# Performance work log

Measured on AMD Instinct MI355X. Metric: run time of the kernel, lower is better.

Reference implementation:

```python
import jax, jax.numpy as jnp
import numpy as np

B, T, D, H = 4, 2048, 1024, 16
DK = D // H  # 64


def setup_inputs() -> dict:
    key = jax.random.key(0)
    ks = jax.random.split(key, 8)
    std = 1.0 / np.sqrt(2.0 * D)  # initialize_weights: normal(0, 1/sqrt(2*d_model*(i_layer+1))), i_layer=0
    inp = {
        "q": jax.random.normal(ks[0], (B, T, D), jnp.float32),
        "k": jax.random.normal(ks[1], (B, T, D), jnp.float32),
        "v": jax.random.normal(ks[2], (B, T, D), jnp.float32),
        "Wq": jax.random.normal(ks[3], (D, D), jnp.float32) * std,
        "Wk": jax.random.normal(ks[4], (D, D), jnp.float32) * std,
        "Wv": jax.random.normal(ks[5], (D, D), jnp.float32) * std,
        "Wo": jax.random.normal(ks[6], (D, D), jnp.float32) * std,
        "bq": jnp.zeros((D,), jnp.float32),
        "bk": jnp.zeros((D,), jnp.float32),
        "bv": jnp.zeros((D,), jnp.float32),
        "bo": jnp.zeros((D,), jnp.float32),
    }
    return inp


def _split_heads(x):
    # (B,T,D) -> (B,H,T,DK), same as x.view(B,T,H,DK).transpose(1,2)
    b, t, _ = x.shape
    return x.reshape(b, t, H, DK).transpose(0, 2, 1, 3)


def reference(q, k, v, Wq, Wk, Wv, Wo, bq, bk, bv, bo):
    # Linear projections (torch Linear: x @ W.T + b)
    qh = _split_heads(q @ Wq.T + bq)  # (B,H,T,DK)
    kh = _split_heads(k @ Wk.T + bk)
    vh = _split_heads(v @ Wv.T + bv)

    # scaled dot-product similarities: (B,H,Tq,Tk)
    scores = jnp.einsum("bhqd,bhkd->bhqk", qh, kh) / jnp.sqrt(jnp.float32(DK))

    # causal mask: tril(ones)==0 positions filled with -inf
    tq, tk = scores.shape[-2], scores.shape[-1]
    causal = jnp.tril(jnp.ones((tq, tk), dtype=bool))
    scores = jnp.where(causal, scores, jnp.float32(-jnp.inf))

    attn = jax.nn.softmax(scores, axis=-1)  # (B,H,Tq,Tk)
    ctx = jnp.einsum("bhqk,bhkd->bhqd", attn, vh)  # (B,H,Tq,DK)

    # merge heads: (B,H,T,DK) -> (B,T,D), then output projection
    merged = ctx.transpose(0, 2, 1, 3).reshape(q.shape[0], tq, D)
    return merged @ Wo.T + bo
```

## Files before the change

kernel.cpp:

```cpp
#include <hip/hip_runtime.h>
#include <hip/hip_bf16.h>
#include <stdint.h>

#define B_ 4
#define T_ 2048
#define D_ 1024
#define H_ 16
#define DK_ 64
#define M_ (B_*T_)

typedef __attribute__((ext_vector_type(8))) short bf16x8;
typedef __attribute__((ext_vector_type(4))) short bf16x4;
typedef __attribute__((ext_vector_type(4))) float f32x4;
typedef __hip_bfloat16 bf16;

__device__ __forceinline__ void gld_lds16(const bf16* g, bf16* l) {
  __builtin_amdgcn_global_load_lds((const __attribute__((address_space(1))) void*)g,
                                   (__attribute__((address_space(3))) void*)l,
                                   16, 0, 0);
}

__device__ __forceinline__ short bfbits(float f) {
  union { bf16 h; short s; } u; u.h = __float2bfloat16(f); return u.s;
}

__global__ __launch_bounds__(256) void cvt_all(
    const float* __restrict__ q, const float* __restrict__ k, const float* __restrict__ v,
    const float* __restrict__ wq, const float* __restrict__ wk,
    const float* __restrict__ wv, const float* __restrict__ wo,
    bf16* __restrict__ qb, bf16* __restrict__ kb, bf16* __restrict__ vb,
    bf16* __restrict__ wqb, bf16* __restrict__ wkb,
    bf16* __restrict__ wvb, bf16* __restrict__ wob) {
  int gid = blockIdx.x * 256 + threadIdx.x;
  const float* src; bf16* dst; int off;
  if (gid < 6291456) {
    int s = gid >> 21; off = gid & 2097151;
    src = (s == 0) ? q : (s == 1) ? k : v;
    dst = (s == 0) ? qb : (s == 1) ? kb : vb;
  } else {
    int g2 = gid - 6291456;
    int s = g2 >> 18; off = g2 & 262143;
    src = (s == 0) ? wq : (s == 1) ? wk : (s == 2) ? wv : wo;
    dst = (s == 0) ? wqb : (s == 1) ? wkb : (s == 2) ? wvb : wob;
  }
  float4 val = reinterpret_cast<const float4*>(src)[off];
  union { ushort4 u; bf16 h[4]; } o;
  o.h[0] = __float2bfloat16(val.x);
  o.h[1] = __float2bfloat16(val.y);
  o.h[2] = __float2bfloat16(val.z);
  o.h[3] = __float2bfloat16(val.w);
  reinterpret_cast<ushort4*>(dst)[off] = o.u;
}

__global__ __launch_bounds__(256) void proj_qkv(
    const bf16* __restrict__ qb, const bf16* __restrict__ kb, const bf16* __restrict__ vb,
    const bf16* __restrict__ Wqb, const bf16* __restrict__ Wkb, const bf16* __restrict__ Wvb,
    const float* __restrict__ bq, const float* __restrict__ bk, const float* __restrict__ bv,
    bf16* __restrict__ Qh, bf16* __restrict__ Kh, bf16* __restrict__ Vt) {
  constexpr int K = 1024;
  constexpr int BK = 64;
  __shared__ __align__(16) bf16 As[128 * BK];
  __shared__ __align__(16) bf16 Bs[128 * BK];

  const int z = blockIdx.z;
  const bool vt = (z == 2);
  const bf16* A  = (z == 0) ? qb : (z == 1) ? kb : Wvb;
  const bf16* Bm = (z == 0) ? Wqb : (z == 1) ? Wkb : vb;
  const float* bias = (z == 0) ? bq : (z == 1) ? bk : bv;
  bf16* out = (z == 0) ? Qh : (z == 1) ? Kh : Vt;
  const float scale = (z == 0) ? 0.125f * 1.4426950408889634f : 1.0f;

  const int bm = vt ? blockIdx.y : blockIdx.x;
  const int bn = vt ? blockIdx.x : blockIdx.y;

  const int tid = threadIdx.x;
  const int w = tid >> 6, l = tid & 63;
  const int wr = w >> 1, wc = w & 1;
  const int lr = l & 15, lk = l >> 4;

  f32x4 acc[4][4] = {};

  for (int k0 = 0; k0 < K; k0 += BK) {
#pragma unroll
    for (int i = 0; i < 4; ++i) {
      int p = i * 256 + tid;
      int row = p >> 3;
      int so = (p & 7) ^ (row & 7);
      gld_lds16(A + (size_t)(bm * 128 + row) * K + k0 + so * 8, &As[p * 8]);
    }
#pragma unroll
    for (int i = 0; i < 4; ++i) {
      int p = i * 256 + tid;
      int row = p >> 3;
      int so = (p & 7) ^ (row & 7);
      gld_lds16(Bm + (size_t)(bn * 128 + row) * K + k0 + so * 8, &Bs[p * 8]);
    }
    __syncthreads();

#pragma unroll
    for (int kk = 0; kk < 2; ++kk) {
      bf16x8 af[4], bfr[4];
#pragma unroll
      for (int m = 0; m < 4; ++m) {
        int row = wr * 64 + m * 16 + lr;
        int slot = (kk * 4 + lk) ^ (row & 7);
        af[m] = *reinterpret_cast<const bf16x8*>(&As[row * BK + slot * 8]);
      }
#pragma unroll
      for (int n = 0; n < 4; ++n) {
        int row = wc * 64 + n * 16 + lr;
        int slot = (kk * 4 + lk) ^ (row & 7);
        bfr[n] = *reinterpret_cast<const bf16x8*>(&Bs[row * BK + slot * 8]);
      }
#pragma unroll
      for (int m = 0; m < 4; ++m)
#pragma unroll
        for (int n = 0; n < 4; ++n)
          acc[m][n] = __builtin_amdgcn_mfma_f32_16x16x32_bf16(af[m], bfr[n], acc[m][n], 0, 0, 0);
    }
    __syncthreads();
  }

  const int crow0 = bm * 128 + wr * 64;
  const int ccol0 = bn * 128 + wc * 64;
#pragma unroll
  for (int m = 0; m < 4; ++m) {
#pragma unroll
    for (int n = 0; n < 4; ++n) {
#pragma unroll
      for (int r = 0; r < 4; ++r) {
        const int row = crow0 + m * 16 + lk * 4 + r;
        const int col = ccol0 + n * 16 + lr;
        if (!vt) {
          float vv = (acc[m][n][r] + bias[col]) * scale;
          size_t idx = (((size_t)(row >> 11) * H_ + (col >> 6)) * T_ + (row & (T_ - 1))) * DK_ + (col & (DK_ - 1));
          out[idx] = __float2bfloat16(vv);
        } else {
          float vv = acc[m][n][r] + bias[row];
          size_t idx = (size_t)(col >> 11) * ((size_t)H_ * DK_ * T_) + (size_t)row * T_ + (col & (T_ - 1));
          out[idx] = __float2bfloat16(vv);
        }
      }
    }
  }
}

__global__ __launch_bounds__(256) void gemm_out(const bf16* __restrict__ A,
                                                const bf16* __restrict__ Bm,
                                                const float* __restrict__ bias,
                                                float* __restrict__ Cout) {
  constexpr int K = 1024;
  constexpr int BK = 64;
  __shared__ __align__(16) bf16 As[128 * BK];
  __shared__ __align__(16) bf16 Bs[128 * BK];

  const int bm = blockIdx.x;
  const int bn = blockIdx.y;
  const int tid = threadIdx.x;
  const int w = tid >> 6, l = tid & 63;
  const int wr = w >> 1, wc = w & 1;
  const int lr = l & 15, lk = l >> 4;

  f32x4 acc[4][4] = {};

  for (int k0 = 0; k0 < K; k0 += BK) {
#pragma unroll
    for (int i = 0; i < 4; ++i) {
      int p = i * 256 + tid;
      int row = p >> 3;
      int so = (p & 7) ^ (row & 7);
      gld_lds16(A + (size_t)(bm * 128 + row) * K + k0 + so * 8, &As[p * 8]);
    }
#pragma unroll
    for (int i = 0; i < 4; ++i) {
      int p = i * 256 + tid;
      int row = p >> 3;
      int so = (p & 7) ^ (row & 7);
      gld_lds16(Bm + (size_t)(bn * 128 + row) * K + k0 + so * 8, &Bs[p * 8]);
    }
    __syncthreads();

#pragma unroll
    for (int kk = 0; kk < 2; ++kk) {
      bf16x8 af[4], bfr[4];
#pragma unroll
      for (int m = 0; m < 4; ++m) {
        int row = wr * 64 + m * 16 + lr;
        int slot = (kk * 4 + lk) ^ (row & 7);
        af[m] = *reinterpret_cast<const bf16x8*>(&As[row * BK + slot * 8]);
      }
#pragma unroll
      for (int n = 0; n < 4; ++n) {
        int row = wc * 64 + n * 16 + lr;
        int slot = (kk * 4 + lk) ^ (row & 7);
        bfr[n] = *reinterpret_cast<const bf16x8*>(&Bs[row * BK + slot * 8]);
      }
#pragma unroll
      for (int m = 0; m < 4; ++m)
#pragma unroll
        for (int n = 0; n < 4; ++n)
          acc[m][n] = __builtin_amdgcn_mfma_f32_16x16x32_bf16(af[m], bfr[n], acc[m][n], 0, 0, 0);
    }
    __syncthreads();
  }

  const int crow0 = bm * 128 + wr * 64;
  const int ccol0 = bn * 128 + wc * 64;
#pragma unroll
  for (int m = 0; m < 4; ++m) {
#pragma unroll
    for (int n = 0; n < 4; ++n) {
#pragma unroll
      for (int r = 0; r < 4; ++r) {
        const int row = crow0 + m * 16 + lk * 4 + r;
        const int col = ccol0 + n * 16 + lr;
        Cout[(size_t)row * D_ + col] = acc[m][n][r] + bias[col];
      }
    }
  }
}

__global__ __launch_bounds__(256, 2) void attn_fwd(const bf16* __restrict__ Qh,
                                                   const bf16* __restrict__ Kh,
                                                   const bf16* __restrict__ Vt,
                                                   bf16* __restrict__ ctx) {
  __shared__ __align__(16) bf16 Kbuf[2][128 * 64];
  __shared__ __align__(16) bf16 Vbuf[2][64 * 128];
  __shared__ __align__(16) char Ps[4][16 * 256];

  const int tid = threadIdx.x, w = tid >> 6, l = tid & 63;
  const int lr = l & 15, lk = l >> 4;
  const int bid = blockIdx.x;
  const int xcd = bid & 7, local = bid >> 3;
  const int hsub = local >> 4;
  const int pp = local & 15;
  char* Pw = &Ps[w][0];

#pragma unroll 1
  for (int ph = 0; ph < 2; ++ph) {
    const int head = xcd * 8 + ph * 4 + hsub;
    const bf16* Qb = Qh + (size_t)head * T_ * DK_;
    const bf16* Kb = Kh + (size_t)head * T_ * DK_;
    const bf16* Vb = Vt + (size_t)head * DK_ * T_;
    const int bb = head >> 4, hh = head & 15;

#pragma unroll 1
    for (int ti = 0; ti < 2; ++ti) {
      const int t = ti ? (31 - pp) : pp;
      const int r0 = t * 64;
      const int ntiles = (t + 2) >> 1;
      const int qrow = r0 + w * 16 + lr;

      const bf16* qp = Qb + (size_t)qrow * DK_ + lk * 8;
      bf16x8 qf0 = *reinterpret_cast<const bf16x8*>(qp);
      bf16x8 qf1 = *reinterpret_cast<const bf16x8*>(qp + 32);

      f32x4 oacc[4] = {};
      float mrow = -1e30f, srow = 0.f;

#pragma unroll
      for (int i = 0; i < 4; ++i) {
        int p = i * 256 + tid;
        int row = p >> 3;
        int so = (p & 7) ^ (row & 7);
        gld_lds16(Kb + (size_t)row * DK_ + so * 8, &Kbuf[0][p * 8]);
      }
#pragma unroll
      for (int i = 0; i < 4; ++i) {
        int p = i * 256 + tid;
        int row = p >> 4;
        int so = (p & 15) ^ (row & 15);
        gld_lds16(Vb + (size_t)row * T_ + so * 8, &Vbuf[0][p * 8]);
      }
      __syncthreads();

      int buf = 0;
#pragma unroll 1
      for (int j = 0; j < ntiles; ++j) {
        const int k0 = j * 128;
        if (j + 1 < ntiles) {
          const int k0n = k0 + 128;
#pragma unroll
          for (int i = 0; i < 4; ++i) {
            int p = i * 256 + tid;
            int row = p >> 3;
            int so = (p & 7) ^ (row & 7);
            gld_lds16(Kb + (size_t)(k0n + row) * DK_ + so * 8, &Kbuf[buf ^ 1][p * 8]);
          }
#pragma unroll
          for (int i = 0; i < 4; ++i) {
            int p = i * 256 + tid;
            int row = p >> 4;
            int so = (p & 15) ^ (row & 15);
            gld_lds16(Vb + (size_t)row * T_ + k0n + so * 8, &Vbuf[buf ^ 1][p * 8]);
          }
        }

        f32x4 sacc[8];
        __builtin_amdgcn_s_setprio(1);
#pragma unroll
        for (int n = 0; n < 8; ++n) {
          int row = n * 16 + lr;
          int s0 = lk ^ (row & 7);
          int s1 = (4 + lk) ^ (row & 7);
          bf16x8 kf0 = *reinterpret_cast<const bf16x8*>(&Kbuf[buf][row * 64 + s0 * 8]);
          bf16x8 kf1 = *reinterpret_cast<const bf16x8*>(&Kbuf[buf][row * 64 + s1 * 8]);
          sacc[n] = f32x4{0.f, 0.f, 0.f, 0.f};
          sacc[n] = __builtin_amdgcn_mfma_f32_16x16x32_bf16(kf0, qf0, sacc[n], 0, 0, 0);
          sacc[n] = __builtin_amdgcn_mfma_f32_16x16x32_bf16(kf1, qf1, sacc[n], 0, 0, 0);
        }
        __builtin_amdgcn_s_setprio(0);

        if (j == ntiles - 1) {
#pragma unroll
          for (int n = 0; n < 8; ++n)
#pragma unroll
            for (int r = 0; r < 4; ++r)
              if (k0 + n * 16 + lk * 4 + r > qrow) sacc[n][r] = -1e30f;
        }

        float pm = -1e30f;
#pragma unroll
        for (int n = 0; n < 8; ++n)
          pm = fmaxf(pm, fmaxf(fmaxf(sacc[n][0], sacc[n][1]), fmaxf(sacc[n][2], sacc[n][3])));
        pm = fmaxf(pm, __shfl_xor(pm, 16, 64));
        pm = fmaxf(pm, __shfl_xor(pm, 32, 64));

        if (!__all(pm - mrow <= 8.0f)) {
          const float mn = fmaxf(mrow, pm);
          const float sc = __builtin_exp2f(mrow - mn);
          mrow = mn;
          srow *= sc;
#pragma unroll
          for (int n = 0; n < 4; ++n)
#pragma unroll
            for (int r = 0; r < 4; ++r)
              oacc[n][r] *= sc;
        }

        float ts = 0.f;
#pragma unroll
        for (int n = 0; n < 8; ++n) {
          float p0 = __builtin_exp2f(sacc[n][0] - mrow);
          float p1 = __builtin_exp2f(sacc[n][1] - mrow);
          float p2 = __builtin_exp2f(sacc[n][2] - mrow);
          float p3 = __builtin_exp2f(sacc[n][3] - mrow);
          ts += (p0 + p1) + (p2 + p3);
          bf16x4 pk;
          pk[0] = bfbits(p0); pk[1] = bfbits(p1); pk[2] = bfbits(p2); pk[3] = bfbits(p3);
          int swz = (n * 2 + (lk >> 1)) ^ (lr & 15);
          *reinterpret_cast<bf16x4*>(Pw + lr * 256 + swz * 16 + (lk & 1) * 8) = pk;
        }
        ts += __shfl_xor(ts, 16, 64);
        ts += __shfl_xor(ts, 32, 64);
        srow += ts;

        bf16x8 pa[4];
#pragma unroll
        for (int kb2 = 0; kb2 < 4; ++kb2) {
          int swz = (kb2 * 4 + lk) ^ (lr & 15);
          pa[kb2] = *reinterpret_cast<const bf16x8*>(Pw + lr * 256 + swz * 16);
        }

        __builtin_amdgcn_s_setprio(1);
#pragma unroll
        for (int n = 0; n < 4; ++n) {
          int row = n * 16 + lr;
#pragma unroll
          for (int kb2 = 0; kb2 < 4; ++kb2) {
            int sl = (kb2 * 4 + lk) ^ (row & 15);
            bf16x8 vf = *reinterpret_cast<const bf16x8*>(&Vbuf[buf][row * 128 + sl * 8]);
            oacc[n] = __builtin_amdgcn_mfma_f32_16x16x32_bf16(vf, pa[kb2], oacc[n], 0, 0, 0);
          }
        }
        __builtin_amdgcn_s_setprio(0);

        __syncthreads();
        buf ^= 1;
      }

      const float inv = 1.0f / srow;
#pragma unroll
      for (int n = 0; n < 4; ++n) {
        bf16x4 pk;
#pragma unroll
        for (int r = 0; r < 4; ++r) pk[r] = bfbits(oacc[n][r] * inv);
        *reinterpret_cast<bf16x4*>(&ctx[((size_t)(bb * T_ + qrow)) * D_ + hh * DK_ + n * 16 + lk * 4]) = pk;
      }
      __syncthreads();
    }
  }
}

extern "C" void kernel_launch(void* const* d_in, const int* in_sizes, int n_in,
                              void* d_out, int out_size, void* d_ws, size_t ws_size,
                              hipStream_t stream) {
  const float* q  = (const float*)d_in[0];
  const float* k  = (const float*)d_in[1];
  const float* v  = (const float*)d_in[2];
  const float* Wq = (const float*)d_in[3];
  const float* Wk = (const float*)d_in[4];
  const float* Wv = (const float*)d_in[5];
  const float* Wo = (const float*)d_in[6];
  const float* bq = (const float*)d_in[7];
  const float* bk = (const float*)d_in[8];
  const float* bv = (const float*)d_in[9];
  const float* bo = (const float*)d_in[10];

  constexpr size_t E_IN = (size_t)M_ * D_;
  constexpr size_t E_W  = (size_t)D_ * D_;
  char* ws = (char*)d_ws;
  size_t off = 0;
  bf16* qb  = (bf16*)(ws + off); off += E_IN * 2;
  bf16* kb  = (bf16*)(ws + off); off += E_IN * 2;
  bf16* vb  = (bf16*)(ws + off); off += E_IN * 2;
  bf16* Wqb = (bf16*)(ws + off); off += E_W * 2;
  bf16* Wkb = (bf16*)(ws + off); off += E_W * 2;
  bf16* Wvb = (bf16*)(ws + off); off += E_W * 2;
  bf16* Wob = (bf16*)(ws + off); off += E_W * 2;
  bf16* Qh  = (bf16*)(ws + off); off += E_IN * 2;
  bf16* Kh  = (bf16*)(ws + off); off += E_IN * 2;
  bf16* Vtw = (bf16*)(ws + off); off += E_IN * 2;
  bf16* ctx = (bf16*)(ws + off); off += E_IN * 2;

  cvt_all<<<dim3(28672), dim3(256), 0, stream>>>(q, k, v, Wq, Wk, Wv, Wo,
                                                 qb, kb, vb, Wqb, Wkb, Wvb, Wob);

  proj_qkv<<<dim3(64, 8, 3), dim3(256), 0, stream>>>(qb, kb, vb, Wqb, Wkb, Wvb,
                                                     bq, bk, bv, Qh, Kh, Vtw);

  attn_fwd<<<dim3(512), dim3(256), 0, stream>>>(Qh, Kh, Vtw, ctx);

  gemm_out<<<dim3(64, 8), dim3(256), 0, stream>>>(ctx, Wob, bo, (float*)d_out);
}
```

Measured before the change: 225.8 us.

## Shrink attention KV tiles to 64 and double grid for higher occupancy

The attention kernel now processes 64-key tiles instead of 128, halving LDS buffers for K, V and P, and raises launch bounds to 4 blocks per CU. The per-block loop over two heads is removed and the grid is doubled to 1024 blocks, with one head per block. The intent is more concurrent waves to hide latency and finer causal masking granularity, at the cost of more loop iterations, barriers and per-tile softmax overhead.

```diff
diff --git a/kernel.cpp b/kernel.cpp
--- a/kernel.cpp
+++ b/kernel.cpp
@@ -220,13 +220,13 @@
   }
 }
 
-__global__ __launch_bounds__(256, 2) void attn_fwd(const bf16* __restrict__ Qh,
+__global__ __launch_bounds__(256, 4) void attn_fwd(const bf16* __restrict__ Qh,
                                                    const bf16* __restrict__ Kh,
                                                    const bf16* __restrict__ Vt,
                                                    bf16* __restrict__ ctx) {
-  __shared__ __align__(16) bf16 Kbuf[2][128 * 64];
-  __shared__ __align__(16) bf16 Vbuf[2][64 * 128];
-  __shared__ __align__(16) char Ps[4][16 * 256];
+  __shared__ __align__(16) bf16 Kbuf[2][64 * 64];
+  __shared__ __align__(16) bf16 Vbuf[2][64 * 64];
+  __shared__ __align__(16) char Ps[4][16 * 128];
 
   const int tid = threadIdx.x, w = tid >> 6, l = tid & 63;
   const int lr = l & 15, lk = l >> 4;
@@ -236,159 +236,138 @@
   const int pp = local & 15;
   char* Pw = &Ps[w][0];
 
+  const int head = xcd * 8 + hsub;
+  const bf16* Qb = Qh + (size_t)head * T_ * DK_;
+  const bf16* Kb = Kh + (size_t)head * T_ * DK_;
+  const bf16* Vb = Vt + (size_t)head * DK_ * T_;
+  const int bb = head >> 4, hh = head & 15;
+
 #pragma unroll 1
-  for (int ph = 0; ph < 2; ++ph) {
-    const int head = xcd * 8 + ph * 4 + hsub;
-    const bf16* Qb = Qh + (size_t)head * T_ * DK_;
-    const bf16* Kb = Kh + (size_t)head * T_ * DK_;
-    const bf16* Vb = Vt + (size_t)head * DK_ * T_;
-    const int bb = head >> 4, hh = head & 15;
-
+  for (int ti = 0; ti < 2; ++ti) {
+    const int t = ti ? (31 - pp) : pp;
+    const int r0 = t * 64;
+    const int ntiles = t + 1;
+    const int qrow = r0 + w * 16 + lr;
+
+    const bf16* qp = Qb + (size_t)qrow * DK_ + lk * 8;
+    bf16x8 qf0 = *reinterpret_cast<const bf16x8*>(qp);
+    bf16x8 qf1 = *reinterpret_cast<const bf16x8*>(qp + 32);
+
+    f32x4 oacc[4] = {};
+    float mrow = -1e30f, srow = 0.f;
+
+#pragma unroll
+    for (int i = 0; i < 2; ++i) {
+      int p = i * 256 + tid;
+      int row = p >> 3;
+      int so = (p & 7) ^ (row & 7);
+      gld_lds16(Kb + (size_t)row * DK_ + so * 8, &Kbuf[0][p * 8]);
+      gld_lds16(Vb + (size_t)row * T_ + so * 8, &Vbuf[0][p * 8]);
+    }
+    __syncthreads();
+
+    int buf = 0;
 #pragma unroll 1
-    for (int ti = 0; ti < 2; ++ti) {
-      const int t = ti ? (31 - pp) : pp;
-      const int r0 = t * 64;
-      const int ntiles = (t + 2) >> 1;
-      const int qrow = r0 + w * 16 + lr;
-
-      const bf16* qp = Qb + (size_t)qrow * DK_ + lk * 8;
-      bf16x8 qf0 = *reinterpret_cast<const bf16x8*>(qp);
-      bf16x8 qf1 = *reinterpret_cast<const bf16x8*>(qp + 32);
-
-      f32x4 oacc[4] = {};
-      float mrow = -1e30f, srow = 0.f;
-
-#pragma unroll
-      for (int i = 0; i < 4; ++i) {
-        int p = i * 256 + tid;
-        int row = p >> 3;
-        int so = (p & 7) ^ (row & 7);
-        gld_lds16(Kb + (size_t)row * DK_ + so * 8, &Kbuf[0][p * 8]);
-      }
-#pragma unroll
-      for (int i = 0; i < 4; ++i) {
-        int p = i * 256 + tid;
-        int row = p >> 4;
-        int so = (p & 15) ^ (row & 15);
-        gld_lds16(Vb + (size_t)row * T_ + so * 8, &Vbuf[0][p * 8]);
-      }
+    for (int j = 0; j < ntiles; ++j) {
+      if (j + 1 < ntiles) {
+        const int k0n = (j + 1) * 64;
+#pragma unroll
+        for (int i = 0; i < 2; ++i) {
+          int p = i * 256 + tid;
+          int row = p >> 3;
+          int so = (p & 7) ^ (row & 7);
+          gld_lds16(Kb + (size_t)(k0n + row) * DK_ + so * 8, &Kbuf[buf ^ 1][p * 8]);
+          gld_lds16(Vb + (size_t)row * T_ + k0n + so * 8, &Vbuf[buf ^ 1][p * 8]);
+        }
+      }
+
+      f32x4 sacc[4] = {};
+      __builtin_amdgcn_s_setprio(1);
+#pragma unroll
+      for (int n = 0; n < 4; ++n) {
+        int row = n * 16 + lr;
+        int s0 = lk ^ (row & 7);
+        int s1 = (4 + lk) ^ (row & 7);
+        bf16x8 kf0 = *reinterpret_cast<const bf16x8*>(&Kbuf[buf][row * 64 + s0 * 8]);
+        bf16x8 kf1 = *reinterpret_cast<const bf16x8*>(&Kbuf[buf][row * 64 + s1 * 8]);
+        sacc[n] = __builtin_amdgcn_mfma_f32_16x16x32_bf16(kf0, qf0, sacc[n], 0, 0, 0);
+        sacc[n] = __builtin_amdgcn_mfma_f32_16x16x32_bf16(kf1, qf1, sacc[n], 0, 0, 0);
+      }
+      __builtin_amdgcn_s_setprio(0);
+
+      if (j == ntiles - 1) {
+#pragma unroll
+        for (int n = 0; n < 4; ++n)
+#pragma unroll
+          for (int r = 0; r < 4; ++r)
+            if (j * 64 + n * 16 + lk * 4 + r > qrow) sacc[n][r] = -1e30f;
+      }
+
+      float pm = fmaxf(fmaxf(sacc[0][0], sacc[0][1]), fmaxf(sacc[0][2], sacc[0][3]));
+#pragma unroll
+      for (int n = 1; n < 4; ++n)
+        pm = fmaxf(pm, fmaxf(fmaxf(sacc[n][0], sacc[n][1]), fmaxf(sacc[n][2], sacc[n][3])));
+      pm = fmaxf(pm, __shfl_xor(pm, 16, 64));
+      pm = fmaxf(pm, __shfl_xor(pm, 32, 64));
+
+      if (!__all(pm - mrow <= 8.0f)) {
+        const float mn = fmaxf(mrow, pm);
+        const float sc = __builtin_exp2f(mrow - mn);
+        mrow = mn;
+        srow *= sc;
+#pragma unroll
+        for (int n = 0; n < 4; ++n)
+#pragma unroll
+          for (int r = 0; r < 4; ++r)
+            oacc[n][r] *= sc;
+      }
+
+      float ts = 0.f;
+#pragma unroll
+      for (int n = 0; n < 4; ++n) {
+        float p0 = __builtin_exp2f(sacc[n][0] - mrow);
+        float p1 = __builtin_exp2f(sacc[n][1] - mrow);
+        float p2 = __builtin_exp2f(sacc[n][2] - mrow);
+        float p3 = __builtin_exp2f(sacc[n][3] - mrow);
+        ts += (p0 + p1) + (p2 + p3);
+        bf16x4 pk;
+        pk[0] = bfbits(p0); pk[1] = bfbits(p1); pk[2] = bfbits(p2); pk[3] = bfbits(p3);
+        int swz = (n * 2 + (lk >> 1)) ^ (lr & 7);
+        *reinterpret_cast<bf16x4*>(Pw + lr * 128 + swz * 16 + (lk & 1) * 8) = pk;
+      }
+      ts += __shfl_xor(ts, 16, 64);
+      ts += __shfl_xor(ts, 32, 64);
+      srow += ts;
+
+      bf16x8 pa0 = *reinterpret_cast<const bf16x8*>(Pw + lr * 128 + ((lk ^ (lr & 7)) << 4));
+      bf16x8 pa1 = *reinterpret_cast<const bf16x8*>(Pw + lr * 128 + (((4 + lk) ^ (lr & 7)) << 4));
+
+      __builtin_amdgcn_s_setprio(1);
+#pragma unroll
+      for (int n = 0; n < 4; ++n) {
+        int row = n * 16 + lr;
+        int s0 = lk ^ (row & 7);
+        int s1 = (4 + lk) ^ (row & 7);
+        bf16x8 vf0 = *reinterpret_cast<const bf16x8*>(&Vbuf[buf][row * 64 + s0 * 8]);
+        bf16x8 vf1 = *reinterpret_cast<const bf16x8*>(&Vbuf[buf][row * 64 + s1 * 8]);
+        oacc[n] = __builtin_amdgcn_mfma_f32_16x16x32_bf16(vf0, pa0, oacc[n], 0, 0, 0);
+        oacc[n] = __builtin_amdgcn_mfma_f32_16x16x32_bf16(vf1, pa1, oacc[n], 0, 0, 0);
+      }
+      __builtin_amdgcn_s_setprio(0);
+
       __syncthreads();
-
-      int buf = 0;
-#pragma unroll 1
-      for (int j = 0; j < ntiles; ++j) {
-        const int k0 = j * 128;
-        if (j + 1 < ntiles) {
-          const int k0n = k0 + 128;
-#pragma unroll
-          for (int i = 0; i < 4; ++i) {
-            int p = i * 256 + tid;
-            int row = p >> 3;
-            int so = (p & 7) ^ (row & 7);
-            gld_lds16(Kb + (size_t)(k0n + row) * DK_ + so * 8, &Kbuf[buf ^ 1][p * 8]);
-          }
-#pragma unroll
-          for (int i = 0; i < 4; ++i) {
-            int p = i * 256 + tid;
-            int row = p >> 4;
-            int so = (p & 15) ^ (row & 15);
-            gld_lds16(Vb + (size_t)row * T_ + k0n + so * 8, &Vbuf[buf ^ 1][p * 8]);
-          }
-        }
-
-        f32x4 sacc[8];
-        __builtin_amdgcn_s_setprio(1);
-#pragma unroll
-        for (int n = 0; n < 8; ++n) {
-          int row = n * 16 + lr;
-          int s0 = lk ^ (row & 7);
-          int s1 = (4 + lk) ^ (row & 7);
-          bf16x8 kf0 = *reinterpret_cast<const bf16x8*>(&Kbuf[buf][row * 64 + s0 * 8]);
-          bf16x8 kf1 = *reinterpret_cast<const bf16x8*>(&Kbuf[buf][row * 64 + s1 * 8]);
-          sacc[n] = f32x4{0.f, 0.f, 0.f, 0.f};
-          sacc[n] = __builtin_amdgcn_mfma_f32_16x16x32_bf16(kf0, qf0, sacc[n], 0, 0, 0);
-          sacc[n] = __builtin_amdgcn_mfma_f32_16x16x32_bf16(kf1, qf1, sacc[n], 0, 0, 0);
-        }
-        __builtin_amdgcn_s_setprio(0);
-
-        if (j == ntiles - 1) {
-#pragma unroll
-          for (int n = 0; n < 8; ++n)
-#pragma unroll
-            for (int r = 0; r < 4; ++r)
-              if (k0 + n * 16 + lk * 4 + r > qrow) sacc[n][r] = -1e30f;
-        }
-
-        float pm = -1e30f;
-#pragma unroll
-        for (int n = 0; n < 8; ++n)
-          pm = fmaxf(pm, fmaxf(fmaxf(sacc[n][0], sacc[n][1]), fmaxf(sacc[n][2], sacc[n][3])));
-        pm = fmaxf(pm, __shfl_xor(pm, 16, 64));
-        pm = fmaxf(pm, __shfl_xor(pm, 32, 64));
-
-        if (!__all(pm - mrow <= 8.0f)) {
-          const float mn = fmaxf(mrow, pm);
-          const float sc = __builtin_exp2f(mrow - mn);
-          mrow = mn;
-          srow *= sc;
-#pragma unroll
-          for (int n = 0; n < 4; ++n)
-#pragma unroll
-            for (int r = 0; r < 4; ++r)
-              oacc[n][r] *= sc;
-        }
-
-        float ts = 0.f;
-#pragma unroll
-        for (int n = 0; n < 8; ++n) {
-          float p0 = __builtin_exp2f(sacc[n][0] - mrow);
-          float p1 = __builtin_exp2f(sacc[n][1] - mrow);
-          float p2 = __builtin_exp2f(sacc[n][2] - mrow);
-          float p3 = __builtin_exp2f(sacc[n][3] - mrow);
-          ts += (p0 + p1) + (p2 + p3);
-          bf16x4 pk;
-          pk[0] = bfbits(p0); pk[1] = bfbits(p1); pk[2] = bfbits(p2); pk[3] = bfbits(p3);
-          int swz = (n * 2 + (lk >> 1)) ^ (lr & 15);
-          *reinterpret_cast<bf16x4*>(Pw + lr * 256 + swz * 16 + (lk & 1) * 8) = pk;
-        }
-        ts += __shfl_xor(ts, 16, 64);
-        ts += __shfl_xor(ts, 32, 64);
-        srow += ts;
-
-        bf16x8 pa[4];
-#pragma unroll
-        for (int kb2 = 0; kb2 < 4; ++kb2) {
-          int swz = (kb2 * 4 + lk) ^ (lr & 15);
-          pa[kb2] = *reinterpret_cast<const bf16x8*>(Pw + lr * 256 + swz * 16);
-        }
-
-        __builtin_amdgcn_s_setprio(1);
-#pragma unroll
-        for (int n = 0; n < 4; ++n) {
-          int row = n * 16 + lr;
-#pragma unroll
-          for (int kb2 = 0; kb2 < 4; ++kb2) {
-            int sl = (kb2 * 4 + lk) ^ (row & 15);
-            bf16x8 vf = *reinterpret_cast<const bf16x8*>(&Vbuf[buf][row * 128 + sl * 8]);
-            oacc[n] = __builtin_amdgcn_mfma_f32_16x16x32_bf16(vf, pa[kb2], oacc[n], 0, 0, 0);
-          }
-        }
-        __builtin_amdgcn_s_setprio(0);
-
-        __syncthreads();
-        buf ^= 1;
-      }
-
-      const float inv = 1.0f / srow;
-#pragma unroll
-      for (int n = 0; n < 4; ++n) {
-        bf16x4 pk;
-#pragma unroll
-        for (int r = 0; r < 4; ++r) pk[r] = bfbits(oacc[n][r] * inv);
-        *reinterpret_cast<bf16x4*>(&ctx[((size_t)(bb * T_ + qrow)) * D_ + hh * DK_ + n * 16 + lk * 4]) = pk;
-      }
-      __syncthreads();
-    }
+      buf ^= 1;
+    }
+
+    const float inv = 1.0f / srow;
+#pragma unroll
+    for (int n = 0; n < 4; ++n) {
+      bf16x4 pk;
+#pragma unroll
+      for (int r = 0; r < 4; ++r) pk[r] = bfbits(oacc[n][r] * inv);
+      *reinterpret_cast<bf16x4*>(&ctx[((size_t)(bb * T_ + qrow)) * D_ + hh * DK_ + n * 16 + lk * 4]) = pk;
+    }
+    __syncthreads();
   }
 }
 
@@ -429,7 +408,7 @@
   proj_qkv<<<dim3(64, 8, 3), dim3(256), 0, stream>>>(qb, kb, vb, Wqb, Wkb, Wvb,
                                                      bq, bk, bv, Qh, Kh, Vtw);
 
-  attn_fwd<<<dim3(512), dim3(256), 0, stream>>>(Qh, Kh, Vtw, ctx);
+  attn_fwd<<<dim3(1024), dim3(256), 0, stream>>>(Qh, Kh, Vtw, ctx);
 
   gemm_out<<<dim3(64, 8), dim3(256), 0, stream>>>(ctx, Wob, bo, (float*)d_out);
 }
```

Result: faster. 221.1 us (-2.1%).
